# Performance work log

Measured on AMD Instinct MI355X. Metric: run time of the kernel, lower is better.

The kernel has to match this reference:

```python
import jax, jax.numpy as jnp
import numpy as np

B, CIN, NF, COUT, H, W = 128, 64, 16, 256, 20, 20


def _warp(features, f):
    # features: (B, Cin, r, c), f: (r, c, 2) flow offsets
    r, c = features.shape[2], features.shape[3]
    grid = jnp.stack(
        jnp.meshgrid(jnp.arange(r, dtype=f.dtype), jnp.arange(c, dtype=f.dtype), indexing='ij'),
        axis=-1,
    )  # (r, c, 2) base index map
    idx = grid + f  # index_map += inverse, inverse == flow[i] after double negation
    base = jnp.floor(idx)
    frac = jax.lax.stop_gradient(idx - base)  # torch detaches s and t
    s, t = frac[..., 0], frac[..., 1]
    b = base.astype(jnp.int32)
    bx, by = b[..., 0], b[..., 1]
    padded = jnp.pad(features, ((0, 0), (0, 0), (1, 1), (1, 1)))  # zero pad by 1

    def gather(ix, iy):
        cx = jnp.clip(ix, 0, r)
        cy = jnp.clip(iy, 0, c)
        return padded[:, :, cx + 1, cy + 1]  # (B, Cin, r, c)

    # NOTE: weight for base_10 is s*(1-t) in the original source (apparent bug,
    # should be (1-s)*t) -- replicated here for faithfulness.
    w00 = (1 - s) * (1 - t)
    w01 = s * (1 - t)
    w10 = s * (1 - t)
    w11 = s * t
    return (gather(bx, by) * w00 + gather(bx + 1, by) * w01
            + gather(bx, by + 1) * w10 + gather(bx + 1, by + 1) * w11)


def setup_inputs() -> dict:
    key = jax.random.key(0)
    k1, k2, k3, k4 = jax.random.split(key, 4)
    x = jax.random.normal(k1, (B, CIN, H, W), dtype=jnp.float32)
    flow = jax.random.normal(k2, (NF, H, W, 2), dtype=jnp.float32)
    combinator = jax.random.normal(k3, (COUT, CIN * NF), dtype=jnp.float32) / np.sqrt(CIN * NF)
    bias = jax.random.normal(k4, (COUT,), dtype=jnp.float32) / np.sqrt(CIN * NF)
    return {"x": x, "flow": flow, "combinator": combinator, "bias": bias}


def reference(x, flow, combinator, bias):
    # per-flow bilinear warp, vectorized over the flow axis
    warped = jax.vmap(lambda f: _warp(x, f))(flow)  # (nf, B, Cin, h, w)
    nf, b, cin, h, w = warped.shape
    # permute(1,3,4,2,0).reshape -> columns ordered channel-major, flow-minor
    feat = warped.transpose(1, 3, 4, 2, 0).reshape(b, h, w, cin * nf)
    out = jnp.einsum('bhwk,ok->bhwo', feat, combinator) + bias
    return out.transpose(0, 3, 1, 2)  # (B, Cout, h, w)
```

## Files before the change

kernel.cpp:

```cpp
#include <hip/hip_runtime.h>
#include <hip/hip_fp16.h>
#include <stdint.h>

#define BATCH 128
#define CIN   64
#define NFLOW 16
#define COUT  256
#define HH    20
#define WW    20
#define NPIX  400
#define KTOT  1024
#define PT    80
#define NPT   5
#define NTH   512
#define FLS   72

typedef __attribute__((ext_vector_type(8))) short sh8;
typedef __attribute__((ext_vector_type(4))) float f4;

__global__ void prep_w(const float* __restrict__ wg, __half* __restrict__ Wf) {
    int gid = blockIdx.x * 256 + threadIdx.x;
    int j8  = gid & 127;
    int row = gid >> 7;
    int kc16 = j8 >> 2;
    int h    = j8 & 3;
    __half* dst = Wf + ((size_t)(kc16 * 16 + (row >> 4)) * 64 + h * 16 + (row & 15)) * 8;
    #pragma unroll
    for (int j = 0; j < 8; ++j) {
        int kp = j8 * 8 + j;
        int kc = kp >> 6;
        int l  = kp & 63;
        int f  = (kc >> 3) * 8 + (l >> 3);
        int c  = (kc & 7) * 8 + (l & 7);
        dst[j] = __float2half(wg[(size_t)row * KTOT + c * NFLOW + f]);
    }
}

__global__ __launch_bounds__(NTH, 4) void flow_main(
    const float* __restrict__ xg, const __half* __restrict__ Wf,
    const float* __restrict__ flowg, const float* __restrict__ biasg,
    float* __restrict__ outg)
{
    __shared__ __align__(16) __half xb[CIN * NPIX];
    __shared__ __align__(16) __half fl[2][PT * FLS];

    const int bid0 = blockIdx.x;
    const int bid  = (bid0 & 7) * (BATCH * NPT / 8) + (bid0 >> 3);
    const int b  = bid / NPT;
    const int pt = bid - b * NPT;
    const int p0 = pt * PT;

    const int tid  = threadIdx.x;
    const int wv   = tid >> 6;
    const int wm   = wv & 3;
    const int wn   = wv >> 2;
    const int lane = tid & 63;
    const int lr   = lane & 15;
    const int lk   = (lane >> 4) * 8;

    const float* xsrc = xg + (size_t)b * (CIN * NPIX);

    #pragma unroll
    for (int it = 0; it < 7; ++it) {
        int idx = it * NTH + tid;
        if (idx < 3200) {
            int cb  = idx / NPIX;
            int pix = idx - cb * NPIX;
            const float* s = xsrc + (size_t)(cb * 8) * NPIX + pix;
            __half2 h0 = __floats2half2_rn(s[0 * NPIX], s[1 * NPIX]);
            __half2 h1 = __floats2half2_rn(s[2 * NPIX], s[3 * NPIX]);
            __half2 h2 = __floats2half2_rn(s[4 * NPIX], s[5 * NPIX]);
            __half2 h3 = __floats2half2_rn(s[6 * NPIX], s[7 * NPIX]);
            uint4 pk;
            pk.x = __builtin_bit_cast(uint32_t, h0);
            pk.y = __builtin_bit_cast(uint32_t, h1);
            pk.z = __builtin_bit_cast(uint32_t, h2);
            pk.w = __builtin_bit_cast(uint32_t, h3);
            *(uint4*)&xb[(size_t)idx * 8] = pk;
        }
    }

    __half2 w2_[2][4];
    int     pb_[2][4];
    int     fo_[2];

    auto build_tables = [&](int fb) {
        #pragma unroll
        for (int gi = 0; gi < 2; ++gi) {
            int g = tid + gi * NTH;
            if (g < PT * 8) {
                int fi = g / PT;
                int p  = g - fi * PT;
                int f  = fb * 8 + fi;
                int gp = p0 + p;
                int i = gp / WW;
                int j = gp - i * WW;
                float fx = flowg[((f * HH + i) * WW + j) * 2 + 0];
                float fy = flowg[((f * HH + i) * WW + j) * 2 + 1];
                float ax = (float)i + fx;
                float ay = (float)j + fy;
                float bxf = floorf(ax), byf = floorf(ay);
                float s = ax - bxf, t = ay - byf;
                int ibx = (int)bxf, iby = (int)byf;
                float w00 = (1.f - s) * (1.f - t);
                float w01 = s * (1.f - t);
                float w10 = s * (1.f - t);
                float w11 = s * t;
                int cx0 = min(max(ibx, 0), HH);
                int cx1 = min(max(ibx + 1, 0), HH);
                int cy0 = min(max(iby, 0), WW);
                int cy1 = min(max(iby + 1, 0), WW);
                int v0 = (cx0 < HH) & (cy0 < WW);
                int v1 = (cx1 < HH) & (cy0 < WW);
                int v2 = (cx0 < HH) & (cy1 < WW);
                int v3 = (cx1 < HH) & (cy1 < WW);
                w2_[gi][0] = __half2half2(__float2half(v0 ? w00 : 0.f));
                w2_[gi][1] = __half2half2(__float2half(v1 ? w01 : 0.f));
                w2_[gi][2] = __half2half2(__float2half(v2 ? w10 : 0.f));
                w2_[gi][3] = __half2half2(__float2half(v3 ? w11 : 0.f));
                pb_[gi][0] = (v0 ? (cx0 * WW + cy0) : 0) * 16;
                pb_[gi][1] = (v1 ? (cx1 * WW + cy0) : 0) * 16;
                pb_[gi][2] = (v2 ? (cx0 * WW + cy1) : 0) * 16;
                pb_[gi][3] = (v3 ? (cx1 * WW + cy1) : 0) * 16;
                fo_[gi] = p * (FLS * 2) + fi * 16;
            }
        }
    };

    build_tables(0);
    __syncthreads();

    f4 acc[4][3] = {};

    for (int kc = 0; kc < 16; ++kc) {
        const int cb = kc & 7;
        if (kc == 8) build_tables(1);

        const sh8* wfp = (const sh8*)Wf + (size_t)(32 * kc + 4 * wm) * 64 + lane;
        sh8 a0_0 = wfp[0],    a0_1 = wfp[64],   a0_2 = wfp[128],  a0_3 = wfp[192];
        sh8 a1_0 = wfp[1024], a1_1 = wfp[1088], a1_2 = wfp[1152], a1_3 = wfp[1216];

        {
            const char* xcb = (const char*)xb + cb * 6400;
            char* flb = (char*)fl[kc & 1];
            #pragma unroll
            for (int gi = 0; gi < 2; ++gi) {
                if (tid + gi * NTH < PT * 8) {
                    __half2 s0 = __builtin_bit_cast(__half2, 0u);
                    __half2 s1 = s0, s2 = s0, s3 = s0;
                    #pragma unroll
                    for (int q = 0; q < 4; ++q) {
                        const uint4 d = *(const uint4*)(xcb + pb_[gi][q]);
                        __half2 wq = w2_[gi][q];
                        s0 = __hfma2(wq, __builtin_bit_cast(__half2, d.x), s0);
                        s1 = __hfma2(wq, __builtin_bit_cast(__half2, d.y), s1);
                        s2 = __hfma2(wq, __builtin_bit_cast(__half2, d.z), s2);
                        s3 = __hfma2(wq, __builtin_bit_cast(__half2, d.w), s3);
                    }
                    uint4 pk;
                    pk.x = __builtin_bit_cast(uint32_t, s0);
                    pk.y = __builtin_bit_cast(uint32_t, s1);
                    pk.z = __builtin_bit_cast(uint32_t, s2);
                    pk.w = __builtin_bit_cast(uint32_t, s3);
                    *(uint4*)(flb + fo_[gi]) = pk;
                }
            }
        }

        __syncthreads();

        const __half* flr = fl[kc & 1];
        __builtin_amdgcn_s_setprio(1);
        if (wn == 0) {
            #pragma unroll
            for (int ni = 0; ni < 2; ++ni) {
                sh8 b0 = *(const sh8*)&flr[(ni * 16 + lr) * FLS + lk];
                acc[0][ni] = __builtin_amdgcn_mfma_f32_16x16x32_f16(a0_0, b0, acc[0][ni], 0, 0, 0);
                acc[1][ni] = __builtin_amdgcn_mfma_f32_16x16x32_f16(a0_1, b0, acc[1][ni], 0, 0, 0);
                acc[2][ni] = __builtin_amdgcn_mfma_f32_16x16x32_f16(a0_2, b0, acc[2][ni], 0, 0, 0);
                acc[3][ni] = __builtin_amdgcn_mfma_f32_16x16x32_f16(a0_3, b0, acc[3][ni], 0, 0, 0);
                sh8 b1 = *(const sh8*)&flr[(ni * 16 + lr) * FLS + 32 + lk];
                acc[0][ni] = __builtin_amdgcn_mfma_f32_16x16x32_f16(a1_0, b1, acc[0][ni], 0, 0, 0);
                acc[1][ni] = __builtin_amdgcn_mfma_f32_16x16x32_f16(a1_1, b1, acc[1][ni], 0, 0, 0);
                acc[2][ni] = __builtin_amdgcn_mfma_f32_16x16x32_f16(a1_2, b1, acc[2][ni], 0, 0, 0);
                acc[3][ni] = __builtin_amdgcn_mfma_f32_16x16x32_f16(a1_3, b1, acc[3][ni], 0, 0, 0);
            }
        } else {
            #pragma unroll
            for (int ni = 0; ni < 3; ++ni) {
                sh8 b0 = *(const sh8*)&flr[((ni + 2) * 16 + lr) * FLS + lk];
                acc[0][ni] = __builtin_amdgcn_mfma_f32_16x16x32_f16(a0_0, b0, acc[0][ni], 0, 0, 0);
                acc[1][ni] = __builtin_amdgcn_mfma_f32_16x16x32_f16(a0_1, b0, acc[1][ni], 0, 0, 0);
                acc[2][ni] = __builtin_amdgcn_mfma_f32_16x16x32_f16(a0_2, b0, acc[2][ni], 0, 0, 0);
                acc[3][ni] = __builtin_amdgcn_mfma_f32_16x16x32_f16(a0_3, b0, acc[3][ni], 0, 0, 0);
                sh8 b1 = *(const sh8*)&flr[((ni + 2) * 16 + lr) * FLS + 32 + lk];
                acc[0][ni] = __builtin_amdgcn_mfma_f32_16x16x32_f16(a1_0, b1, acc[0][ni], 0, 0, 0);
                acc[1][ni] = __builtin_amdgcn_mfma_f32_16x16x32_f16(a1_1, b1, acc[1][ni], 0, 0, 0);
                acc[2][ni] = __builtin_amdgcn_mfma_f32_16x16x32_f16(a1_2, b1, acc[2][ni], 0, 0, 0);
                acc[3][ni] = __builtin_amdgcn_mfma_f32_16x16x32_f16(a1_3, b1, acc[3][ni], 0, 0, 0);
            }
        }
        __builtin_amdgcn_s_setprio(0);
    }

    float* ob = outg + (size_t)b * (COUT * NPIX) + p0;
    #pragma unroll
    for (int mi = 0; mi < 4; ++mi) {
        #pragma unroll
        for (int r = 0; r < 4; ++r) {
            int m = wm * 64 + mi * 16 + (lane >> 4) * 4 + r;
            float bs = biasg[m];
            if (wn == 0) {
                #pragma unroll
                for (int ni = 0; ni < 2; ++ni)
                    ob[(size_t)m * NPIX + ni * 16 + lr] = acc[mi][ni][r] + bs;
            } else {
                #pragma unroll
                for (int ni = 0; ni < 3; ++ni)
                    ob[(size_t)m * NPIX + (ni + 2) * 16 + lr] = acc[mi][ni][r] + bs;
            }
        }
    }
}

extern "C" void kernel_launch(void* const* d_in, const int* in_sizes, int n_in,
                              void* d_out, int out_size, void* d_ws, size_t ws_size,
                              hipStream_t stream) {
    const float* x    = (const float*)d_in[0];
    const float* flow = (const float*)d_in[1];
    const float* comb = (const float*)d_in[2];
    const float* bias = (const float*)d_in[3];
    float* out = (float*)d_out;

    __half* Wf = (__half*)d_ws;

    prep_w<<<dim3(128), dim3(256), 0, stream>>>(comb, Wf);
    flow_main<<<dim3(BATCH * NPT), dim3(NTH), 0, stream>>>(x, Wf, flow, bias, out);
}
```

Before: 56.99 us.

## Software-pipeline warp fill with MFMA and repartition waves to cover all pixels

Warping of the next channel chunk into the alternate shared buffer now runs while the current chunk's MFMAs execute, leaving one barrier per iteration instead of serialising fill and compute. The wave-to-output split also changes: each wave now owns 32 output channels across all 80 pixels, instead of 64 channels across 2 or 3 pixel tiles. That loads fewer A fragments per wave and removes the unbalanced wn branch. Table building is regrouped so each wave handles one flow with lanes over pixels, leaving lanes 16-63 idle in the second pass. It is moved to kc==7 so the tables are ready when fill(8) needs them.

```diff
diff --git a/kernel.cpp b/kernel.cpp
--- a/kernel.cpp
+++ b/kernel.cpp
@@ -52,8 +52,6 @@
 
     const int tid  = threadIdx.x;
     const int wv   = tid >> 6;
-    const int wm   = wv & 3;
-    const int wn   = wv >> 2;
     const int lane = tid & 63;
     const int lr   = lane & 15;
     const int lk   = (lane >> 4) * 8;
@@ -86,12 +84,10 @@
 
     auto build_tables = [&](int fb) {
         #pragma unroll
-        for (int gi = 0; gi < 2; ++gi) {
-            int g = tid + gi * NTH;
-            if (g < PT * 8) {
-                int fi = g / PT;
-                int p  = g - fi * PT;
-                int f  = fb * 8 + fi;
+        for (int it = 0; it < 2; ++it) {
+            if (it == 0 || lane < 16) {
+                int p  = it * 64 + lane;
+                int f  = fb * 8 + wv;
                 int gp = p0 + p;
                 int i = gp / WW;
                 int j = gp - i * WW;
@@ -114,111 +110,90 @@
                 int v1 = (cx1 < HH) & (cy0 < WW);
                 int v2 = (cx0 < HH) & (cy1 < WW);
                 int v3 = (cx1 < HH) & (cy1 < WW);
-                w2_[gi][0] = __half2half2(__float2half(v0 ? w00 : 0.f));
-                w2_[gi][1] = __half2half2(__float2half(v1 ? w01 : 0.f));
-                w2_[gi][2] = __half2half2(__float2half(v2 ? w10 : 0.f));
-                w2_[gi][3] = __half2half2(__float2half(v3 ? w11 : 0.f));
-                pb_[gi][0] = (v0 ? (cx0 * WW + cy0) : 0) * 16;
-                pb_[gi][1] = (v1 ? (cx1 * WW + cy0) : 0) * 16;
-                pb_[gi][2] = (v2 ? (cx0 * WW + cy1) : 0) * 16;
-                pb_[gi][3] = (v3 ? (cx1 * WW + cy1) : 0) * 16;
-                fo_[gi] = p * (FLS * 2) + fi * 16;
+                w2_[it][0] = __half2half2(__float2half(v0 ? w00 : 0.f));
+                w2_[it][1] = __half2half2(__float2half(v1 ? w01 : 0.f));
+                w2_[it][2] = __half2half2(__float2half(v2 ? w10 : 0.f));
+                w2_[it][3] = __half2half2(__float2half(v3 ? w11 : 0.f));
+                pb_[it][0] = (v0 ? (cx0 * WW + cy0) : 0) * 16;
+                pb_[it][1] = (v1 ? (cx1 * WW + cy0) : 0) * 16;
+                pb_[it][2] = (v2 ? (cx0 * WW + cy1) : 0) * 16;
+                pb_[it][3] = (v3 ? (cx1 * WW + cy1) : 0) * 16;
+                fo_[it] = p * (FLS * 2) + wv * 16;
+            }
+        }
+    };
+
+    auto fill = [&](int kc) {
+        const char* xcb = (const char*)xb + (kc & 7) * 6400;
+        char* flb = (char*)fl[kc & 1];
+        #pragma unroll
+        for (int it = 0; it < 2; ++it) {
+            if (it == 0 || lane < 16) {
+                __half2 s0 = __builtin_bit_cast(__half2, 0u);
+                __half2 s1 = s0, s2 = s0, s3 = s0;
+                #pragma unroll
+                for (int q = 0; q < 4; ++q) {
+                    const uint4 d = *(const uint4*)(xcb + pb_[it][q]);
+                    __half2 wq = w2_[it][q];
+                    s0 = __hfma2(wq, __builtin_bit_cast(__half2, d.x), s0);
+                    s1 = __hfma2(wq, __builtin_bit_cast(__half2, d.y), s1);
+                    s2 = __hfma2(wq, __builtin_bit_cast(__half2, d.z), s2);
+                    s3 = __hfma2(wq, __builtin_bit_cast(__half2, d.w), s3);
+                }
+                uint4 pk;
+                pk.x = __builtin_bit_cast(uint32_t, s0);
+                pk.y = __builtin_bit_cast(uint32_t, s1);
+                pk.z = __builtin_bit_cast(uint32_t, s2);
+                pk.w = __builtin_bit_cast(uint32_t, s3);
+                *(uint4*)(flb + fo_[it]) = pk;
             }
         }
     };
 
     build_tables(0);
     __syncthreads();
-
-    f4 acc[4][3] = {};
+    fill(0);
+    __syncthreads();
+
+    f4 acc[2][5] = {};
 
     for (int kc = 0; kc < 16; ++kc) {
-        const int cb = kc & 7;
-        if (kc == 8) build_tables(1);
-
-        const sh8* wfp = (const sh8*)Wf + (size_t)(32 * kc + 4 * wm) * 64 + lane;
-        sh8 a0_0 = wfp[0],    a0_1 = wfp[64],   a0_2 = wfp[128],  a0_3 = wfp[192];
-        sh8 a1_0 = wfp[1024], a1_1 = wfp[1088], a1_2 = wfp[1152], a1_3 = wfp[1216];
-
-        {
-            const char* xcb = (const char*)xb + cb * 6400;
-            char* flb = (char*)fl[kc & 1];
-            #pragma unroll
-            for (int gi = 0; gi < 2; ++gi) {
-                if (tid + gi * NTH < PT * 8) {
-                    __half2 s0 = __builtin_bit_cast(__half2, 0u);
-                    __half2 s1 = s0, s2 = s0, s3 = s0;
-                    #pragma unroll
-                    for (int q = 0; q < 4; ++q) {
-                        const uint4 d = *(const uint4*)(xcb + pb_[gi][q]);
-                        __half2 wq = w2_[gi][q];
-                        s0 = __hfma2(wq, __builtin_bit_cast(__half2, d.x), s0);
-                        s1 = __hfma2(wq, __builtin_bit_cast(__half2, d.y), s1);
-                        s2 = __hfma2(wq, __builtin_bit_cast(__half2, d.z), s2);
-                        s3 = __hfma2(wq, __builtin_bit_cast(__half2, d.w), s3);
-                    }
-                    uint4 pk;
-                    pk.x = __builtin_bit_cast(uint32_t, s0);
-                    pk.y = __builtin_bit_cast(uint32_t, s1);
-                    pk.z = __builtin_bit_cast(uint32_t, s2);
-                    pk.w = __builtin_bit_cast(uint32_t, s3);
-                    *(uint4*)(flb + fo_[gi]) = pk;
-                }
-            }
-        }
-
-        __syncthreads();
+        if (kc == 7) build_tables(1);
+
+        const sh8* wfp = (const sh8*)Wf + (size_t)(2 * kc * 16 + 2 * wv) * 64 + lane;
+        sh8 a00 = wfp[0];
+        sh8 a01 = wfp[64];
+        sh8 a10 = wfp[1024];
+        sh8 a11 = wfp[1088];
+
+        if (kc < 15) fill(kc + 1);
 
         const __half* flr = fl[kc & 1];
         __builtin_amdgcn_s_setprio(1);
-        if (wn == 0) {
-            #pragma unroll
-            for (int ni = 0; ni < 2; ++ni) {
-                sh8 b0 = *(const sh8*)&flr[(ni * 16 + lr) * FLS + lk];
-                acc[0][ni] = __builtin_amdgcn_mfma_f32_16x16x32_f16(a0_0, b0, acc[0][ni], 0, 0, 0);
-                acc[1][ni] = __builtin_amdgcn_mfma_f32_16x16x32_f16(a0_1, b0, acc[1][ni], 0, 0, 0);
-                acc[2][ni] = __builtin_amdgcn_mfma_f32_16x16x32_f16(a0_2, b0, acc[2][ni], 0, 0, 0);
-                acc[3][ni] = __builtin_amdgcn_mfma_f32_16x16x32_f16(a0_3, b0, acc[3][ni], 0, 0, 0);
-                sh8 b1 = *(const sh8*)&flr[(ni * 16 + lr) * FLS + 32 + lk];
-                acc[0][ni] = __builtin_amdgcn_mfma_f32_16x16x32_f16(a1_0, b1, acc[0][ni], 0, 0, 0);
-                acc[1][ni] = __builtin_amdgcn_mfma_f32_16x16x32_f16(a1_1, b1, acc[1][ni], 0, 0, 0);
-                acc[2][ni] = __builtin_amdgcn_mfma_f32_16x16x32_f16(a1_2, b1, acc[2][ni], 0, 0, 0);
-                acc[3][ni] = __builtin_amdgcn_mfma_f32_16x16x32_f16(a1_3, b1, acc[3][ni], 0, 0, 0);
-            }
-        } else {
-            #pragma unroll
-            for (int ni = 0; ni < 3; ++ni) {
-                sh8 b0 = *(const sh8*)&flr[((ni + 2) * 16 + lr) * FLS + lk];
-                acc[0][ni] = __builtin_amdgcn_mfma_f32_16x16x32_f16(a0_0, b0, acc[0][ni], 0, 0, 0);
-                acc[1][ni] = __builtin_amdgcn_mfma_f32_16x16x32_f16(a0_1, b0, acc[1][ni], 0, 0, 0);
-                acc[2][ni] = __builtin_amdgcn_mfma_f32_16x16x32_f16(a0_2, b0, acc[2][ni], 0, 0, 0);
-                acc[3][ni] = __builtin_amdgcn_mfma_f32_16x16x32_f16(a0_3, b0, acc[3][ni], 0, 0, 0);
-                sh8 b1 = *(const sh8*)&flr[((ni + 2) * 16 + lr) * FLS + 32 + lk];
-                acc[0][ni] = __builtin_amdgcn_mfma_f32_16x16x32_f16(a1_0, b1, acc[0][ni], 0, 0, 0);
-                acc[1][ni] = __builtin_amdgcn_mfma_f32_16x16x32_f16(a1_1, b1, acc[1][ni], 0, 0, 0);
-                acc[2][ni] = __builtin_amdgcn_mfma_f32_16x16x32_f16(a1_2, b1, acc[2][ni], 0, 0, 0);
-                acc[3][ni] = __builtin_amdgcn_mfma_f32_16x16x32_f16(a1_3, b1, acc[3][ni], 0, 0, 0);
-            }
+        #pragma unroll
+        for (int nf = 0; nf < 5; ++nf) {
+            sh8 b0 = *(const sh8*)&flr[(nf * 16 + lr) * FLS + lk];
+            acc[0][nf] = __builtin_amdgcn_mfma_f32_16x16x32_f16(a00, b0, acc[0][nf], 0, 0, 0);
+            acc[1][nf] = __builtin_amdgcn_mfma_f32_16x16x32_f16(a01, b0, acc[1][nf], 0, 0, 0);
+            sh8 b1 = *(const sh8*)&flr[(nf * 16 + lr) * FLS + 32 + lk];
+            acc[0][nf] = __builtin_amdgcn_mfma_f32_16x16x32_f16(a10, b1, acc[0][nf], 0, 0, 0);
+            acc[1][nf] = __builtin_amdgcn_mfma_f32_16x16x32_f16(a11, b1, acc[1][nf], 0, 0, 0);
         }
         __builtin_amdgcn_s_setprio(0);
+
+        __syncthreads();
     }
 
     float* ob = outg + (size_t)b * (COUT * NPIX) + p0;
     #pragma unroll
-    for (int mi = 0; mi < 4; ++mi) {
+    for (int mi = 0; mi < 2; ++mi) {
         #pragma unroll
         for (int r = 0; r < 4; ++r) {
-            int m = wm * 64 + mi * 16 + (lane >> 4) * 4 + r;
+            int m = (wv * 2 + mi) * 16 + (lane >> 4) * 4 + r;
             float bs = biasg[m];
-            if (wn == 0) {
-                #pragma unroll
-                for (int ni = 0; ni < 2; ++ni)
-                    ob[(size_t)m * NPIX + ni * 16 + lr] = acc[mi][ni][r] + bs;
-            } else {
-                #pragma unroll
-                for (int ni = 0; ni < 3; ++ni)
-                    ob[(size_t)m * NPIX + (ni + 2) * 16 + lr] = acc[mi][ni][r] + bs;
-            }
+            #pragma unroll
+            for (int nf = 0; nf < 5; ++nf)
+                ob[(size_t)m * NPIX + nf * 16 + lr] = acc[mi][nf][r] + bs;
         }
     }
 }
```

Measured after the change: 55.62 us. 2.4% less time.
